# Kernel tuning notes

Measured on AMD Instinct MI355X. Metric: run time of the kernel, lower is better.

## Reference

```python
import jax, jax.numpy as jnp
import numpy as np

N_NODES = 20000
N_EDGES = 320000
NS = 16      # input scalar channels (0e)
NVH = 16     # hidden vector channels (1o)
STEPS = 3
BLOCKS = 2
SQRT3 = 3.0 ** 0.5  # component-normalized Y1


def _tp(xs, xv, ys, yv):
    """Tensor product of (0e,1o) features with (0e,1o) attrs, keeping 0e and 1o outputs.
    xs:[n,a] xv:[n,b,3] ys:[n,c] yv:[n,d,3] -> ts:[n,a*c+b*d], tv:[n,a*d+b*c,3]"""
    n = xs.shape[0]
    ss = jnp.einsum('na,nc->nac', xs, ys).reshape(n, -1)          # 0e x 0e -> 0e
    vv = jnp.einsum('nbi,ndi->nbd', xv, yv).reshape(n, -1)        # 1o . 1o -> 0e
    ts = jnp.concatenate([ss, vv], axis=-1)
    sv = jnp.einsum('na,ndi->nadi', xs, yv).reshape(n, -1, 3)     # 0e x 1o -> 1o
    vs = jnp.einsum('nbi,nc->nbci', xv, ys).reshape(n, -1, 3)     # 1o x 0e -> 1o
    tv = jnp.concatenate([sv, vs], axis=1)
    return ts, tv


def _tplg(xs, xv, ys, yv, Ws, bs, Wv, out_v):
    """TensorProductLinearGate: tensor product -> Linear -> gate (sigmoid gates on vectors, gelu on scalars)."""
    ts, tv = _tp(xs, xv, ys, yv)
    s = ts @ Ws + bs                                  # [n, out_v (gates) + out_s]
    v = jnp.einsum('npi,pq->nqi', tv, Wv)             # [n, out_v, 3]
    gates = jax.nn.sigmoid(s[:, :out_v])
    feat = jax.nn.gelu(s[:, out_v:])
    return feat, v * gates[:, :, None]


def _seg_mean(x, idx, n):
    s = jax.ops.segment_sum(x, idx, num_segments=n)
    cnt = jax.ops.segment_sum(jnp.ones((idx.shape[0],), x.dtype), idx, num_segments=n)
    return s / jnp.maximum(cnt, 1.0).reshape((n,) + (1,) * (x.ndim - 1))


def setup_inputs() -> dict:
    key = jax.random.key(0)
    ks = jax.random.split(key, 20)

    def w(k, shape):
        return jax.random.normal(k, shape, jnp.float32) / np.sqrt(shape[-2]).astype(np.float32)

    return {
        'node_scalars': jax.random.normal(ks[0], (N_NODES, NS), jnp.float32),
        'node_pos': jax.random.normal(ks[1], (N_NODES, 1, 3), jnp.float32),
        'senders': jax.random.randint(ks[2], (N_EDGES,), 0, N_NODES, jnp.int32),
        'receivers': jax.random.randint(ks[3], (N_EDGES,), 0, N_NODES, jnp.int32),
        'eWs0': w(ks[4], (STEPS, 34, 32)),
        'ebs0': jnp.zeros((STEPS, 32), jnp.float32),
        'eWv0': w(ks[5], (STEPS, 34, NVH)),
        'eWs1': w(ks[6], (STEPS, 32, 32)),
        'ebs1': jnp.zeros((STEPS, 32), jnp.float32),
        'eWv1': w(ks[7], (STEPS, 32, NVH)),
        'nWs': w(ks[8], (STEPS, BLOCKS, 289, 17)),
        'nbs': jnp.zeros((STEPS, BLOCKS, 17), jnp.float32),
        'nWv': w(ks[9], (STEPS, BLOCKS, 289, 1)),
        'fWs': w(ks[10], (STEPS, NS, NS)),
        'fbs': jnp.zeros((STEPS, NS), jnp.float32),
        'fWv': w(ks[11], (STEPS, 1, 1)),
    }


def reference(node_scalars, node_pos, senders, receivers, eWs0, ebs0, eWv0,
              eWs1, ebs1, eWv1, nWs, nbs, nWv, fWs, fbs, fWv):
    s, v = node_scalars, node_pos                      # [N,16], [N,1,3]
    N = s.shape[0]
    E = senders.shape[0]
    inv = 1.0 / (E - 1)                                # normalize_messages
    for t in range(STEPS):
        # --- edge update ---
        r = v[senders, 0] - v[receivers, 0]            # r_ij = x_i - x_j
        rhat = r / (jnp.linalg.norm(r, axis=-1, keepdims=True) + 1e-8)
        a_s = jnp.ones((E, 1), s.dtype)                # Y0 (component norm)
        a_v = (SQRT3 * rhat)[:, None, :]               # Y1 (component norm)
        xs = jnp.concatenate([s[senders], s[receivers]], axis=-1)
        xv = jnp.concatenate([v[senders], v[receivers]], axis=1)
        ms, mv = _tplg(xs, xv, a_s, a_v, eWs0[t], ebs0[t], eWv0[t], NVH)
        ms, mv = _tplg(ms, mv, a_s, a_v, eWs1[t], ebs1[t], eWv1[t], NVH)
        # --- aggregate (segment mean to receivers) + message normalization ---
        ys = jnp.concatenate([_seg_mean(ms, receivers, N), _seg_mean(a_s, receivers, N)], axis=-1) * inv
        yv = jnp.concatenate([_seg_mean(mv, receivers, N), _seg_mean(a_v, receivers, N)], axis=1) * inv
        # --- node update ---
        ns_, nv_ = s, v
        for b in range(BLOCKS):
            ns_, nv_ = _tplg(ns_, nv_, ys, yv, nWs[t, b], nbs[t, b], nWv[t, b], 1)
        # --- Linear back to irreps_in + residual ---
        s = s + ns_ @ fWs[t] + fbs[t]
        v = v + jnp.einsum('npi,pq->nqi', nv_, fWv[t])
    return jnp.concatenate([s, v.reshape(N, 3)], axis=-1)  # [N, 19]
```

## Files before the change

kernel.cpp:

```cpp
#include <hip/hip_runtime.h>

#define N_NODES 20000
#define N_EDGES 320000
#define CH 68

__device__ __forceinline__ float sigm(float x) { return 1.0f / (1.0f + __expf(-x)); }
__device__ __forceinline__ float gelu(float x) {
    return x * sigm(1.5957691216057308f * (x + 0.044715f * x * x * x));
}

__global__ void init_kernel(const float* __restrict__ s0, const float* __restrict__ p0,
                            float* __restrict__ s, float4* __restrict__ v4,
                            float* __restrict__ cnt) {
    int idx = blockIdx.x * 256 + threadIdx.x;
    if (idx < N_NODES * 16) s[idx] = s0[idx];
    if (idx < N_NODES) {
        v4[idx] = make_float4(p0[idx * 3], p0[idx * 3 + 1], p0[idx * 3 + 2], 0.f);
        cnt[idx] = 0.f;
    }
}

__global__ void count_kernel(const int* __restrict__ rcv, float* __restrict__ cnt) {
    int e = blockIdx.x * 256 + threadIdx.x;
    if (e < N_EDGES) unsafeAtomicAdd(&cnt[rcv[e]], 1.0f);
}

__global__ __launch_bounds__(1024) void scan_kernel(const float* __restrict__ cnt,
                                                    int* __restrict__ offs,
                                                    int* __restrict__ cursor) {
    __shared__ int sdata[1024];
    const int t = threadIdx.x;
    const int base = t * 20;
    int local[20];
    int sum = 0;
#pragma unroll
    for (int k = 0; k < 20; k++) {
        const int n = base + k;
        const int c = (n < N_NODES) ? (int)cnt[n] : 0;
        local[k] = sum;
        sum += c;
    }
    sdata[t] = sum;
    __syncthreads();
    for (int d = 1; d < 1024; d <<= 1) {
        const int v = (t >= d) ? sdata[t - d] : 0;
        __syncthreads();
        sdata[t] += v;
        __syncthreads();
    }
    const int pre = (t == 0) ? 0 : sdata[t - 1];
#pragma unroll
    for (int k = 0; k < 20; k++) {
        const int n = base + k;
        if (n < N_NODES) {
            offs[n] = pre + local[k];
            cursor[n] = 0;
        }
    }
}

__global__ void scatter_kernel(const int* __restrict__ rcv, const int* __restrict__ offs,
                               int* __restrict__ cursor, int* __restrict__ perm) {
    int e = blockIdx.x * 256 + threadIdx.x;
    if (e < N_EDGES) {
        const int n = rcv[e];
        const int slot = offs[n] + atomicAdd(&cursor[n], 1);
        perm[slot] = e;
    }
}

__global__ __launch_bounds__(256) void edge_compute_kernel(
    const float4* __restrict__ s4, const float4* __restrict__ v4,
    const int* __restrict__ snd, const int* __restrict__ rcv,
    const int* __restrict__ perm,
    const float* __restrict__ Ws0, const float* __restrict__ bs0, const float* __restrict__ Wv0,
    const float* __restrict__ Ws1, const float* __restrict__ bs1, const float* __restrict__ Wv1,
    float* __restrict__ msg) {
    __shared__ float lW[3168];
    const int tid = threadIdx.x;
    {
        for (int idx = tid; idx < 1088; idx += 256) lW[idx] = Ws0[idx];
        for (int idx = tid; idx < 544; idx += 256) lW[1088 + idx] = Wv0[idx];
        for (int idx = tid; idx < 1024; idx += 256) lW[1632 + idx] = Ws1[idx];
        for (int idx = tid; idx < 512; idx += 256) lW[2656 + idx] = Wv1[idx];
    }
    __syncthreads();
    const float* __restrict__ lWs0 = lW;
    const float* __restrict__ lWv0 = lW + 1088;
    const float* __restrict__ lWs1 = lW + 1632;
    const float* __restrict__ lWv1 = lW + 2656;

    const int e = blockIdx.x * 256 + tid;
    const int eid = perm[e];
    const int i = snd[eid], j = rcv[eid];

    const float4 vi4 = v4[i], vj4 = v4[j];
    const float vi0 = vi4.x, vi1 = vi4.y, vi2 = vi4.z;
    const float vj0 = vj4.x, vj1 = vj4.y, vj2 = vj4.z;
    const float r0 = vi0 - vj0, r1 = vi1 - vj1, r2 = vi2 - vj2;
    const float nrm = sqrtf(r0 * r0 + r1 * r1 + r2 * r2);
    const float scl = 1.7320508075688772f / (nrm + 1e-8f);
    const float a0 = r0 * scl, a1 = r1 * scl, a2 = r2 * scl;

    float xs[32];
    {
        float4 A = s4[i * 4 + 0], B = s4[i * 4 + 1], C = s4[i * 4 + 2], D = s4[i * 4 + 3];
        xs[0] = A.x; xs[1] = A.y; xs[2] = A.z; xs[3] = A.w;
        xs[4] = B.x; xs[5] = B.y; xs[6] = B.z; xs[7] = B.w;
        xs[8] = C.x; xs[9] = C.y; xs[10] = C.z; xs[11] = C.w;
        xs[12] = D.x; xs[13] = D.y; xs[14] = D.z; xs[15] = D.w;
        A = s4[j * 4 + 0]; B = s4[j * 4 + 1]; C = s4[j * 4 + 2]; D = s4[j * 4 + 3];
        xs[16] = A.x; xs[17] = A.y; xs[18] = A.z; xs[19] = A.w;
        xs[20] = B.x; xs[21] = B.y; xs[22] = B.z; xs[23] = B.w;
        xs[24] = C.x; xs[25] = C.y; xs[26] = C.z; xs[27] = C.w;
        xs[28] = D.x; xs[29] = D.y; xs[30] = D.z; xs[31] = D.w;
    }
    const float di = vi0 * a0 + vi1 * a1 + vi2 * a2;
    const float dj = vj0 * a0 + vj1 * a1 + vj2 * a2;

    float sl[32];
#pragma unroll
    for (int o = 0; o < 32; o++) sl[o] = bs0[o] + di * lWs0[32 * 32 + o] + dj * lWs0[33 * 32 + o];
#pragma unroll
    for (int p = 0; p < 32; p++) {
        const float x = xs[p];
#pragma unroll
        for (int o = 0; o < 32; o++) sl[o] += x * lWs0[p * 32 + o];
    }
    float al[16];
#pragma unroll
    for (int q = 0; q < 16; q++) al[q] = 0.f;
#pragma unroll
    for (int p = 0; p < 32; p++) {
        const float x = xs[p];
#pragma unroll
        for (int q = 0; q < 16; q++) al[q] += x * lWv0[p * 16 + q];
    }
    float ms[16], mv0[16], mv1[16], mv2[16];
#pragma unroll
    for (int q = 0; q < 16; q++) {
        const float g = sigm(sl[q]);
        const float w32 = lWv0[32 * 16 + q], w33 = lWv0[33 * 16 + q];
        mv0[q] = (al[q] * a0 + w32 * vi0 + w33 * vj0) * g;
        mv1[q] = (al[q] * a1 + w32 * vi1 + w33 * vj1) * g;
        mv2[q] = (al[q] * a2 + w32 * vi2 + w33 * vj2) * g;
    }
#pragma unroll
    for (int p = 0; p < 16; p++) ms[p] = gelu(sl[16 + p]);

    float sl2[32];
#pragma unroll
    for (int o = 0; o < 32; o++) sl2[o] = bs1[o];
#pragma unroll
    for (int p = 0; p < 16; p++) {
        const float x = ms[p];
#pragma unroll
        for (int o = 0; o < 32; o++) sl2[o] += x * lWs1[p * 32 + o];
    }
#pragma unroll
    for (int q = 0; q < 16; q++) {
        const float x = mv0[q] * a0 + mv1[q] * a1 + mv2[q] * a2;
#pragma unroll
        for (int o = 0; o < 32; o++) sl2[o] += x * lWs1[(16 + q) * 32 + o];
    }

    float4* mrow = (float4*)(msg + (size_t)e * CH);
    mrow[0] = make_float4(gelu(sl2[16]), gelu(sl2[17]), gelu(sl2[18]), gelu(sl2[19]));
    mrow[1] = make_float4(gelu(sl2[20]), gelu(sl2[21]), gelu(sl2[22]), gelu(sl2[23]));
    mrow[2] = make_float4(gelu(sl2[24]), gelu(sl2[25]), gelu(sl2[26]), gelu(sl2[27]));
    mrow[3] = make_float4(gelu(sl2[28]), gelu(sl2[29]), gelu(sl2[30]), gelu(sl2[31]));
#pragma unroll
    for (int qg = 0; qg < 4; qg++) {
        float t[12];
#pragma unroll
        for (int qq = 0; qq < 4; qq++) {
            const int q = qg * 4 + qq;
            const float g = sigm(sl2[q]);
            float be = 0.f;
#pragma unroll
            for (int p = 0; p < 16; p++) be += ms[p] * lWv1[p * 16 + q];
            float u0 = be * a0, u1 = be * a1, u2 = be * a2;
#pragma unroll
            for (int p = 0; p < 16; p++) {
                const float w = lWv1[(16 + p) * 16 + q];
                u0 += mv0[p] * w; u1 += mv1[p] * w; u2 += mv2[p] * w;
            }
            t[qq * 3 + 0] = u0 * g;
            t[qq * 3 + 1] = u1 * g;
            t[qq * 3 + 2] = u2 * g;
        }
        mrow[4 + qg * 3 + 0] = make_float4(t[0], t[1], t[2], t[3]);
        mrow[4 + qg * 3 + 1] = make_float4(t[4], t[5], t[6], t[7]);
        mrow[4 + qg * 3 + 2] = make_float4(t[8], t[9], t[10], t[11]);
    }
    mrow[16] = make_float4(a0, a1, a2, 0.f);
}

__global__ __launch_bounds__(256, 2) void node_kernel(
    float* __restrict__ s, float4* __restrict__ v4,
    const float* __restrict__ msg, const int* __restrict__ offs,
    const float* __restrict__ cntb,
    const float* __restrict__ nWs, const float* __restrict__ nbs, const float* __restrict__ nWv,
    const float* __restrict__ fWs, const float* __restrict__ fbs, const float* __restrict__ fWv,
    float* __restrict__ out) {
    __shared__ float nsl[64 * 17];
    __shared__ float u[21 * 256];
    __shared__ float lw[289 * 17 + 289];
    __shared__ float lf[256];
    const int tid = threadIdx.x;
    const int lane = tid & 63;
    const int w = tid >> 6;
    const int n0 = blockIdx.x * 64 + lane;
    const bool valid = n0 < N_NODES;
    const int n = valid ? n0 : 0;
    const float inv = 1.0f / 319999.0f;

    if (tid < 256) lf[tid] = fWs[tid];

    {
        const int nl = tid >> 2;
        const int q = tid & 3;
        const int gn0 = blockIdx.x * 64 + nl;
        const int gn = (gn0 < N_NODES) ? gn0 : 0;
        const int o0 = offs[gn];
        const int deg = (gn0 < N_NODES) ? (int)cntb[gn] : 0;
        float4 acc0 = make_float4(0.f, 0.f, 0.f, 0.f);
        float4 acc1 = acc0, acc2 = acc0, acc3 = acc0, acc4 = acc0;
        for (int r = 0; r < deg; r++) {
            const float4* row = (const float4*)(msg + (size_t)(o0 + r) * CH);
            const float4 t0 = row[q];
            const float4 t1 = row[q + 4];
            const float4 t2 = row[q + 8];
            const float4 t3 = row[q + 12];
            acc0.x += t0.x; acc0.y += t0.y; acc0.z += t0.z; acc0.w += t0.w;
            acc1.x += t1.x; acc1.y += t1.y; acc1.z += t1.z; acc1.w += t1.w;
            acc2.x += t2.x; acc2.y += t2.y; acc2.z += t2.z; acc2.w += t2.w;
            acc3.x += t3.x; acc3.y += t3.y; acc3.z += t3.z; acc3.w += t3.w;
            if (q == 0) {
                const float4 t4 = row[16];
                acc4.x += t4.x; acc4.y += t4.y; acc4.z += t4.z; acc4.w += t4.w;
            }
        }
        float4* rowl = (float4*)(u + nl * CH);
        rowl[q] = acc0;
        rowl[q + 4] = acc1;
        rowl[q + 8] = acc2;
        rowl[q + 12] = acc3;
        if (q == 0) rowl[16] = acc4;
    }
    __syncthreads();

    const float cnt = cntb[n];
    const float f = inv / fmaxf(cnt, 1.0f);
    const float* ag = u + lane * CH;
    const int c0 = w * 4;
    const bool w3 = (w == 3);

    float yso[4];
#pragma unroll
    for (int k = 0; k < 4; k++) yso[k] = ag[c0 + k] * f;
    const float ys16 = cnt * f;
    float yvo[4][3];
#pragma unroll
    for (int k = 0; k < 4; k++) {
        const int d = c0 + k;
        yvo[k][0] = ag[16 + d * 3 + 0] * f;
        yvo[k][1] = ag[16 + d * 3 + 1] * f;
        yvo[k][2] = ag[16 + d * 3 + 2] * f;
    }
    float yv16[3] = {ag[64] * f, ag[65] * f, ag[66] * f};
    const float4 nvv = v4[n];
    float nv0 = nvv.x, nv1 = nvv.y, nv2 = nvv.z;

    if (w == 0) {
        const float4* srow = (const float4*)(s + n * 16);
        const float4 A = srow[0], B = srow[1], C = srow[2], D = srow[3];
        float* p = nsl + lane * 17;
        p[0] = A.x; p[1] = A.y; p[2] = A.z; p[3] = A.w;
        p[4] = B.x; p[5] = B.y; p[6] = B.z; p[7] = B.w;
        p[8] = C.x; p[9] = C.y; p[10] = C.z; p[11] = C.w;
        p[12] = D.x; p[13] = D.y; p[14] = D.z; p[15] = D.w;
    }

    float nsreg[16];
#pragma unroll 1
    for (int b = 0; b < 2; b++) {
        for (int idx = tid; idx < 289 * 17; idx += 256) lw[idx] = nWs[b * 289 * 17 + idx];
        for (int idx = tid; idx < 289; idx += 256) lw[289 * 17 + idx] = nWv[b * 289 + idx];
        __syncthreads();
        const float* W = lw;
        const float* Wv = lw + 289 * 17;
        const float* bb = nbs + b * 17;
        float* part = u;
        float acc[17];
#pragma unroll
        for (int o = 0; o < 17; o++) acc[o] = (w == 0) ? bb[o] : 0.f;
        float gam[4] = {0.f, 0.f, 0.f, 0.f};
        float gam16 = 0.f;
#pragma unroll 2
        for (int a = 0; a < 16; a++) {
            const float xa = nsl[lane * 17 + a];
            const float* Wa = W + (a * 17 + c0) * 17;
#pragma unroll
            for (int k = 0; k < 4; k++) {
                const float cf = xa * yso[k];
#pragma unroll
                for (int o = 0; o < 17; o++) acc[o] += cf * Wa[k * 17 + o];
            }
            const float* Wva = Wv + a * 17 + c0;
#pragma unroll
            for (int k = 0; k < 4; k++) gam[k] += xa * Wva[k];
            if (w3) {
                const float cf = xa * ys16;
                const float* W16 = W + (a * 17 + 16) * 17;
#pragma unroll
                for (int o = 0; o < 17; o++) acc[o] += cf * W16[o];
                gam16 += xa * Wv[a * 17 + 16];
            }
        }
#pragma unroll
        for (int k = 0; k < 4; k++) {
            const int d = c0 + k;
            const float cf = nv0 * yvo[k][0] + nv1 * yvo[k][1] + nv2 * yvo[k][2];
            const float* Wp = W + (272 + d) * 17;
#pragma unroll
            for (int o = 0; o < 17; o++) acc[o] += cf * Wp[o];
        }
        if (w3) {
            const float cf = nv0 * yv16[0] + nv1 * yv16[1] + nv2 * yv16[2];
            const float* Wp = W + (272 + 16) * 17;
#pragma unroll
            for (int o = 0; o < 17; o++) acc[o] += cf * Wp[o];
        }
        float vl0 = 0.f, vl1 = 0.f, vl2 = 0.f, sc2 = 0.f;
#pragma unroll
        for (int k = 0; k < 4; k++) {
            vl0 += gam[k] * yvo[k][0]; vl1 += gam[k] * yvo[k][1]; vl2 += gam[k] * yvo[k][2];
            sc2 += yso[k] * Wv[272 + c0 + k];
        }
        if (w3) {
            vl0 += gam16 * yv16[0]; vl1 += gam16 * yv16[1]; vl2 += gam16 * yv16[2];
            sc2 += ys16 * Wv[272 + 16];
        }
#pragma unroll
        for (int o = 0; o < 17; o++) part[o * 256 + tid] = acc[o];
        part[17 * 256 + tid] = vl0;
        part[18 * 256 + tid] = vl1;
        part[19 * 256 + tid] = vl2;
        part[20 * 256 + tid] = sc2;
        __syncthreads();
        float tot[21];
#pragma unroll
        for (int t = 0; t < 21; t++)
            tot[t] = part[t * 256 + lane] + part[t * 256 + 64 + lane] +
                     part[t * 256 + 128 + lane] + part[t * 256 + 192 + lane];
        const float g = sigm(tot[0]);
#pragma unroll
        for (int a = 0; a < 16; a++) nsreg[a] = gelu(tot[1 + a]);
        const float nx = (tot[17] + tot[20] * nv0) * g;
        const float ny = (tot[18] + tot[20] * nv1) * g;
        const float nz = (tot[19] + tot[20] * nv2) * g;
        nv0 = nx; nv1 = ny; nv2 = nz;
        if (b == 0 && w == 0) {
            float* p = nsl + lane * 17;
#pragma unroll
            for (int a = 0; a < 16; a++) p[a] = nsreg[a];
        }
        __syncthreads();
    }
    float so[16];
#pragma unroll
    for (int a = 0; a < 16; a++) so[a] = fbs[a];
#pragma unroll
    for (int p = 0; p < 16; p++) {
        const float x = nsreg[p];
#pragma unroll
        for (int a = 0; a < 16; a++) so[a] += x * lf[p * 16 + a];
    }
    if (valid && w == 0) {
        const float fw = fWv[0];
        float sn[16];
#pragma unroll
        for (int a = 0; a < 16; a++) { sn[a] = s[n * 16 + a] + so[a]; }
#pragma unroll
        for (int a = 0; a < 16; a++) s[n * 16 + a] = sn[a];
        const float w0o = nvv.x + nv0 * fw;
        const float w1o = nvv.y + nv1 * fw;
        const float w2o = nvv.z + nv2 * fw;
        v4[n] = make_float4(w0o, w1o, w2o, 0.f);
        if (out) {
#pragma unroll
            for (int a = 0; a < 16; a++) out[n * 19 + a] = sn[a];
            out[n * 19 + 16] = w0o;
            out[n * 19 + 17] = w1o;
            out[n * 19 + 18] = w2o;
        }
    }
}

extern "C" void kernel_launch(void* const* d_in, const int* in_sizes, int n_in,
                              void* d_out, int out_size, void* d_ws, size_t ws_size,
                              hipStream_t stream) {
    const float* node_scalars = (const float*)d_in[0];
    const float* node_pos = (const float*)d_in[1];
    const int* senders = (const int*)d_in[2];
    const int* receivers = (const int*)d_in[3];
    const float* eWs0 = (const float*)d_in[4];
    const float* ebs0 = (const float*)d_in[5];
    const float* eWv0 = (const float*)d_in[6];
    const float* eWs1 = (const float*)d_in[7];
    const float* ebs1 = (const float*)d_in[8];
    const float* eWv1 = (const float*)d_in[9];
    const float* nWs = (const float*)d_in[10];
    const float* nbs = (const float*)d_in[11];
    const float* nWv = (const float*)d_in[12];
    const float* fWs = (const float*)d_in[13];
    const float* fbs = (const float*)d_in[14];
    const float* fWv = (const float*)d_in[15];

    float* ws = (float*)d_ws;
    float* s = ws;
    float* v = s + N_NODES * 16;
    float* cnt = v + N_NODES * 4;
    int* offs = (int*)(cnt + N_NODES);
    int* cursor = offs + N_NODES;
    int* perm = cursor + N_NODES;
    float* msg = (float*)(perm + N_EDGES);
    float* out = (float*)d_out;
    float4* v4 = (float4*)v;

    init_kernel<<<(N_NODES * 16 + 255) / 256, 256, 0, stream>>>(node_scalars, node_pos, s, v4, cnt);
    count_kernel<<<(N_EDGES + 255) / 256, 256, 0, stream>>>(receivers, cnt);
    scan_kernel<<<1, 1024, 0, stream>>>(cnt, offs, cursor);
    scatter_kernel<<<(N_EDGES + 255) / 256, 256, 0, stream>>>(receivers, offs, cursor, perm);
    for (int t = 0; t < 3; t++) {
        edge_compute_kernel<<<N_EDGES / 256, 256, 0, stream>>>(
            (const float4*)s, (const float4*)v4, senders, receivers, perm,
            eWs0 + t * 34 * 32, ebs0 + t * 32, eWv0 + t * 34 * 16,
            eWs1 + t * 32 * 32, ebs1 + t * 32, eWv1 + t * 32 * 16,
            msg);
        node_kernel<<<(N_NODES + 63) / 64, 256, 0, stream>>>(
            s, v4, msg, offs, cnt,
            nWs + t * 2 * 289 * 17, nbs + t * 2 * 17, nWv + t * 2 * 289,
            fWs + t * 256, fbs + t * 16, fWv + t,
            (t == 2) ? out : nullptr);
    }
}
```

Before: 581.0 us.

## Aggregate edge directions per receiver in-wavefront instead of storing per-edge

Measured after the change: 713.4 us. +22.8%, slower.

```diff
diff --git a/kernel.cpp b/kernel.cpp
--- a/kernel.cpp
+++ b/kernel.cpp
@@ -3,6 +3,7 @@
 #define N_NODES 20000
 #define N_EDGES 320000
 #define CH 68
+#define MSGF 64
 
 __device__ __forceinline__ float sigm(float x) { return 1.0f / (1.0f + __expf(-x)); }
 __device__ __forceinline__ float gelu(float x) {
@@ -75,7 +76,7 @@
     const int* __restrict__ perm,
     const float* __restrict__ Ws0, const float* __restrict__ bs0, const float* __restrict__ Wv0,
     const float* __restrict__ Ws1, const float* __restrict__ bs1, const float* __restrict__ Wv1,
-    float* __restrict__ msg) {
+    float* __restrict__ msg, float* __restrict__ agg3) {
     __shared__ float lW[3168];
     const int tid = threadIdx.x;
     {
@@ -101,6 +102,25 @@
     const float nrm = sqrtf(r0 * r0 + r1 * r1 + r2 * r2);
     const float scl = 1.7320508075688772f / (nrm + 1e-8f);
     const float a0 = r0 * scl, a1 = r1 * scl, a2 = r2 * scl;
+
+    {
+        const int lane = tid & 63;
+        int cur = __shfl(j, 0);
+        float acc = 0.f;
+#pragma unroll 4
+        for (int k = 0; k < 64; k++) {
+            const int jj = __shfl(j, k);
+            const float b0 = __shfl(a0, k), b1 = __shfl(a1, k), b2 = __shfl(a2, k);
+            const float b = (lane == 0) ? b0 : ((lane == 1) ? b1 : b2);
+            if (jj != cur) {
+                if (lane < 3) unsafeAtomicAdd(&agg3[cur * 4 + lane], acc);
+                acc = 0.f;
+                cur = jj;
+            }
+            acc += b;
+        }
+        if (lane < 3) unsafeAtomicAdd(&agg3[cur * 4 + lane], acc);
+    }
 
     float xs[32];
     {
@@ -164,7 +184,7 @@
         for (int o = 0; o < 32; o++) sl2[o] += x * lWs1[(16 + q) * 32 + o];
     }
 
-    float4* mrow = (float4*)(msg + (size_t)e * CH);
+    float4* mrow = (float4*)(msg + (size_t)e * MSGF);
     mrow[0] = make_float4(gelu(sl2[16]), gelu(sl2[17]), gelu(sl2[18]), gelu(sl2[19]));
     mrow[1] = make_float4(gelu(sl2[20]), gelu(sl2[21]), gelu(sl2[22]), gelu(sl2[23]));
     mrow[2] = make_float4(gelu(sl2[24]), gelu(sl2[25]), gelu(sl2[26]), gelu(sl2[27]));
@@ -193,16 +213,15 @@
         mrow[4 + qg * 3 + 1] = make_float4(t[4], t[5], t[6], t[7]);
         mrow[4 + qg * 3 + 2] = make_float4(t[8], t[9], t[10], t[11]);
     }
-    mrow[16] = make_float4(a0, a1, a2, 0.f);
 }
 
 __global__ __launch_bounds__(256, 2) void node_kernel(
     float* __restrict__ s, float4* __restrict__ v4,
     const float* __restrict__ msg, const int* __restrict__ offs,
-    const float* __restrict__ cntb,
+    const float* __restrict__ cntb, float* __restrict__ agg3,
     const float* __restrict__ nWs, const float* __restrict__ nbs, const float* __restrict__ nWv,
     const float* __restrict__ fWs, const float* __restrict__ fbs, const float* __restrict__ fWv,
-    float* __restrict__ out) {
+    float* __restrict__ out, int zero_agg) {
     __shared__ float nsl[64 * 17];
     __shared__ float u[21 * 256];
     __shared__ float lw[289 * 17 + 289];
@@ -225,9 +244,9 @@
         const int o0 = offs[gn];
         const int deg = (gn0 < N_NODES) ? (int)cntb[gn] : 0;
         float4 acc0 = make_float4(0.f, 0.f, 0.f, 0.f);
-        float4 acc1 = acc0, acc2 = acc0, acc3 = acc0, acc4 = acc0;
+        float4 acc1 = acc0, acc2 = acc0, acc3 = acc0;
         for (int r = 0; r < deg; r++) {
-            const float4* row = (const float4*)(msg + (size_t)(o0 + r) * CH);
+            const float4* row = (const float4*)(msg + (size_t)(o0 + r) * MSGF);
             const float4 t0 = row[q];
             const float4 t1 = row[q + 4];
             const float4 t2 = row[q + 8];
@@ -236,17 +255,12 @@
             acc1.x += t1.x; acc1.y += t1.y; acc1.z += t1.z; acc1.w += t1.w;
             acc2.x += t2.x; acc2.y += t2.y; acc2.z += t2.z; acc2.w += t2.w;
             acc3.x += t3.x; acc3.y += t3.y; acc3.z += t3.z; acc3.w += t3.w;
-            if (q == 0) {
-                const float4 t4 = row[16];
-                acc4.x += t4.x; acc4.y += t4.y; acc4.z += t4.z; acc4.w += t4.w;
-            }
         }
         float4* rowl = (float4*)(u + nl * CH);
         rowl[q] = acc0;
         rowl[q + 4] = acc1;
         rowl[q + 8] = acc2;
         rowl[q + 12] = acc3;
-        if (q == 0) rowl[16] = acc4;
     }
     __syncthreads();
 
@@ -268,7 +282,7 @@
         yvo[k][1] = ag[16 + d * 3 + 1] * f;
         yvo[k][2] = ag[16 + d * 3 + 2] * f;
     }
-    float yv16[3] = {ag[64] * f, ag[65] * f, ag[66] * f};
+    float yv16[3] = {agg3[n * 4 + 0] * f, agg3[n * 4 + 1] * f, agg3[n * 4 + 2] * f};
     const float4 nvv = v4[n];
     float nv0 = nvv.x, nv1 = nvv.y, nv2 = nvv.z;
 
@@ -394,6 +408,10 @@
             out[n * 19 + 16] = w0o;
             out[n * 19 + 17] = w1o;
             out[n * 19 + 18] = w2o;
+        }
+        if (zero_agg) {
+            float4* az = (float4*)(agg3 + n * 4);
+            *az = make_float4(0.f, 0.f, 0.f, 0.f);
         }
     }
 }
@@ -425,7 +443,8 @@
     int* offs = (int*)(cnt + N_NODES);
     int* cursor = offs + N_NODES;
     int* perm = cursor + N_NODES;
-    float* msg = (float*)(perm + N_EDGES);
+    float* agg3 = (float*)(perm + N_EDGES);
+    float* msg = agg3 + N_NODES * 4;
     float* out = (float*)d_out;
     float4* v4 = (float4*)v;
 
@@ -433,16 +452,17 @@
     count_kernel<<<(N_EDGES + 255) / 256, 256, 0, stream>>>(receivers, cnt);
     scan_kernel<<<1, 1024, 0, stream>>>(cnt, offs, cursor);
     scatter_kernel<<<(N_EDGES + 255) / 256, 256, 0, stream>>>(receivers, offs, cursor, perm);
+    hipMemsetAsync(agg3, 0, (size_t)N_NODES * 4 * sizeof(float), stream);
     for (int t = 0; t < 3; t++) {
         edge_compute_kernel<<<N_EDGES / 256, 256, 0, stream>>>(
             (const float4*)s, (const float4*)v4, senders, receivers, perm,
             eWs0 + t * 34 * 32, ebs0 + t * 32, eWv0 + t * 34 * 16,
             eWs1 + t * 32 * 32, ebs1 + t * 32, eWv1 + t * 32 * 16,
-            msg);
+            msg, agg3);
         node_kernel<<<(N_NODES + 63) / 64, 256, 0, stream>>>(
-            s, v4, msg, offs, cnt,
+            s, v4, msg, offs, cnt, agg3,
             nWs + t * 2 * 289 * 17, nbs + t * 2 * 17, nWv + t * 2 * 289,
             fWs + t * 256, fbs + t * 16, fWv + t,
-            (t == 2) ? out : nullptr);
-    }
-}
+            (t == 2) ? out : nullptr, (t < 2) ? 1 : 0);
+    }
+}
```
